# Kernel tuning notes

Measured on AMD Instinct MI355X. Metric: run time of the kernel, lower is better.

## Reference

```python
import jax, jax.numpy as jnp
import numpy as np

MARGIN = 0.36
ALPHA_INIT = 0.0
ALPHA_MOMENT = 0.995
LAMBDA_CLEAN = 1.0
LAMBDA_ADV = 1.0
EPS_SIM = 0.01
BIG = 99999.0

CNT = 8192
DIM = 128


def dot_to_dist(dot, alpha, eps=1e-12):
    return alpha * (1.0 - dot) + (1.0 - alpha) * jnp.sqrt(2.0 * (1.0 - dot) + eps)


def find_hard_negatives(dmat):
    # HyNet-style mining: dmat[i, j] = 'distance' between a_i and p_j.
    # Positive pair is the diagonal; hardest negative for triplet i is the min
    # over row i (a_i vs other p) or column i (p_i vs other a), diag excluded.
    cnt = dmat.shape[0]
    dm = dmat + jnp.eye(cnt, dtype=dmat.dtype) * BIG  # mask diagonal
    row_min = dm.min(axis=1)
    row_arg = jnp.argmin(dm, axis=1)
    col_min = dm.min(axis=0)
    col_arg = jnp.argmin(dm, axis=0)
    idx_a = jnp.arange(cnt)
    idx_p = idx_a + cnt
    # indices into cat([a, p]): hardest p lives at j+cnt, hardest a at j
    idx_n = jnp.where(row_min < col_min, row_arg + cnt, col_arg)
    return idx_a, idx_p, idx_n


def estimate_alpha(dots, labels, weights):
    # Vectorized over the 200-point alpha grid (original: Python loop).
    alphas = jnp.arange(-1.0, 1.0, 0.01, dtype=dots.dtype)  # [K=200]
    one_minus = (1.0 - dots)[None, :]                        # [1, N]
    sq = jnp.sqrt(2.0 * (1.0 - dots) + 1e-12)[None, :]       # [1, N]
    dists = alphas[:, None] * one_minus + (1.0 - alphas)[:, None] * sq  # [K, N]
    n = dists.shape[1]
    mean = dists.mean(axis=1, keepdims=True)
    std = jnp.sqrt(((dists - mean) ** 2).sum(axis=1, keepdims=True) / (n - 1))  # unbiased, as torch.std
    probs = jax.nn.sigmoid(-(dists - mean) / std)
    bce = jnp.mean(-labels * jnp.log(probs) * weights
                   - (1.0 - labels) * jnp.log(1.0 - probs) * weights, axis=1)  # [K]
    return alphas[jnp.argmin(bce)]


def _rowdot(x, y):
    return jnp.sum(x * y, axis=1)


def setup_inputs() -> dict:
    key = jax.random.key(0)
    k1, k2, k3 = jax.random.split(key, 3)
    descs = jax.random.normal(k1, (6 * CNT, DIM), dtype=jnp.float32)
    l_a_adv = jax.random.uniform(k2, (CNT,), dtype=jnp.float32)
    l_p_adv = jax.random.uniform(k3, (CNT,), dtype=jnp.float32)
    return {"descs": descs, "l_a_adv": l_a_adv, "l_p_adv": l_p_adv}


def reference(descs, l_a_adv, l_p_adv):
    cnt = descs.shape[0] // 6
    xn = descs / jnp.linalg.norm(descs, axis=1, keepdims=True)
    a     = xn[0 * cnt:1 * cnt]
    p     = xn[1 * cnt:2 * cnt]
    a_rec = xn[2 * cnt:3 * cnt]
    p_rec = xn[3 * cnt:4 * cnt]
    a_adv = xn[4 * cnt:5 * cnt]
    p_adv = xn[5 * cnt:6 * cnt]

    # hard-negative mining (no_grad in original)
    sg = jax.lax.stop_gradient
    smat_ap   = sg(a)     @ sg(p).T       # [cnt, cnt]
    smat_arpa = sg(a_rec) @ sg(p_adv).T
    smat_aapr = sg(a_adv) @ sg(p_rec).T
    idx_a, idx_p, idx_n                = find_hard_negatives(1.0 / smat_ap + EPS_SIM)
    idx_a_arpa, idx_p_arpa, idx_n_arpa = find_hard_negatives(1.0 / smat_arpa + EPS_SIM)
    idx_a_aapr, idx_p_aapr, idx_n_aapr = find_hard_negatives(1.0 / smat_aapr + EPS_SIM)

    xn_ap   = jnp.concatenate([a, p], axis=0)
    xn_arpa = jnp.concatenate([a_rec, p_adv], axis=0)
    xn_aapr = jnp.concatenate([a_adv, p_rec], axis=0)

    pos_ap   = _rowdot(xn_ap[idx_a],        xn_ap[idx_p])
    neg_ap   = _rowdot(xn_ap[idx_a],        xn_ap[idx_n])
    pos_arpa = _rowdot(xn_arpa[idx_a_arpa], xn_arpa[idx_p_arpa])
    neg_arpa = _rowdot(xn_arpa[idx_a_arpa], xn_arpa[idx_n_arpa])
    pos_aapr = _rowdot(xn_aapr[idx_a_aapr], xn_aapr[idx_p_aapr])
    neg_aapr = _rowdot(xn_aapr[idx_a_aapr], xn_aapr[idx_n_aapr])

    acos = lambda d: jnp.arccos(jnp.clip(d, -1.0, 1.0))
    mask = (MARGIN + acos(pos_ap) - acos(neg_ap) > 0).astype(descs.dtype)

    # alpha estimation (no_grad)
    dots = sg(jnp.concatenate([pos_ap, pos_arpa, pos_aapr, neg_ap, neg_arpa, neg_aapr]))
    labels = jnp.concatenate([jnp.ones(cnt * 3, descs.dtype), jnp.zeros(cnt * 3, descs.dtype)])
    weights = jnp.concatenate([
        jnp.full((cnt,), LAMBDA_CLEAN, descs.dtype), jnp.full((2 * cnt,), LAMBDA_ADV, descs.dtype),
        jnp.full((cnt,), LAMBDA_CLEAN, descs.dtype), jnp.full((2 * cnt,), LAMBDA_ADV, descs.dtype)])
    alpha_opt = estimate_alpha(dots, labels, weights)
    alpha = ALPHA_INIT * ALPHA_MOMENT + alpha_opt * (1.0 - ALPHA_MOMENT)

    loss_triplet_clean = jnp.mean((dot_to_dist(pos_ap, alpha) - dot_to_dist(neg_ap, alpha)) * mask) * LAMBDA_CLEAN
    loss_triplet_arpa = jnp.mean((l_p_adv * dot_to_dist(pos_arpa, alpha) - dot_to_dist(neg_arpa, alpha)) * mask) * LAMBDA_ADV
    loss_triplet_aapr = jnp.mean((l_a_adv * dot_to_dist(pos_aapr, alpha) - dot_to_dist(neg_aapr, alpha)) * mask) * LAMBDA_ADV
    loss = jnp.mean(jnp.stack([loss_triplet_clean, loss_triplet_arpa, loss_triplet_aapr]))

    l_mean = (l_a_adv.mean() + l_p_adv.mean()) / 2.0
    mask_ratio = mask.sum() / cnt
    return (loss, loss_triplet_clean, loss_triplet_arpa, loss_triplet_aapr, l_mean, alpha, alpha_opt, mask_ratio)
```

## Files before the change

### kernel.cpp

```cpp
#include <hip/hip_runtime.h>
#include <stdint.h>

#define CNT 8192
#define DIM 128

typedef unsigned int u32;

#define OFF_POS     ((size_t)0)
#define OFF_NEG     (OFF_POS + (size_t)3*CNT*4)
#define OFF_ROWPART (OFF_NEG + (size_t)3*CNT*4)
#define OFF_COLPART (OFF_ROWPART + (size_t)3*64*CNT*4)
#define OFF_RNORM   (OFF_COLPART + (size_t)3*64*CNT*4)
#define OFF_U       (OFF_RNORM + (size_t)6*CNT*4)
#define OFF_V       (OFF_U + (size_t)6*CNT*4)
#define OFF_MPART   (OFF_V + (size_t)6*CNT*4)
#define OFF_PSUM    (OFF_MPART + (size_t)4096)
#define OFF_XNB     (OFF_PSUM + (size_t)192*200*4)

typedef __attribute__((ext_vector_type(8))) short short8;
typedef __attribute__((ext_vector_type(4))) float f32x4;

__device__ __forceinline__ float fract1(float x){
#if __has_builtin(__builtin_amdgcn_fractf)
  return __builtin_amdgcn_fractf(x);
#else
  return x - floorf(x);
#endif
}
__device__ __forceinline__ u32 umax2(u32 a, u32 b){ return a > b ? a : b; }
__device__ __forceinline__ u32 umax3(u32 a, u32 b, u32 c){ u32 t = a > b ? a : b; return t > c ? t : c; }
__device__ __forceinline__ u32 umin2(u32 a, u32 b){ return a < b ? a : b; }

__device__ __forceinline__ float block_sum(float x, float* red, int tid){
  #pragma unroll
  for (int m=1;m<64;m<<=1) x += __shfl_xor(x, m, 64);
  if ((tid & 63) == 0) red[tid>>6] = x;
  __syncthreads();
  const float r = red[0]+red[1]+red[2]+red[3];
  __syncthreads();
  return r;
}

__global__ __launch_bounds__(256) void knorm(const float* __restrict__ in,
                                             unsigned int* __restrict__ xnb32,
                                             float* __restrict__ rnorm){
  const int row  = blockIdx.x*4 + (threadIdx.x>>6);
  const int lane = threadIdx.x & 63;
  const float2 v = *(const float2*)(in + (size_t)row*DIM + lane*2);
  float ss = v.x*v.x + v.y*v.y;
  #pragma unroll
  for (int m=1;m<64;m<<=1) ss += __shfl_xor(ss, m, 64);
  const float rn = 1.0f / sqrtf(ss);
  const float sc = ((row & CNT) ? 1.0f : 0.25f) * rn;
  unsigned int ux = __float_as_uint(v.x*sc), uy = __float_as_uint(v.y*sc);
  ux = (ux + 0x7FFFu + ((ux>>16)&1u)) >> 16;
  uy = (uy + 0x7FFFu + ((uy>>16)&1u)) >> 16;
  xnb32[(size_t)row*64 + lane] = ux | (uy<<16);
  if (lane == 0) rnorm[row] = rn;
}

__global__ __launch_bounds__(256) void kgemm(const unsigned short* __restrict__ xnb,
    u32* __restrict__ rowpart, u32* __restrict__ colpart){
  __shared__ __align__(16) unsigned short S[4][128*32];
  const int pair = blockIdx.z;
  const int xo3[3] = {0, 2*CNT, 4*CNT};
  const int yo3[3] = {CNT, 5*CNT, 3*CNT};
  const unsigned short* __restrict__ X = xnb + (size_t)xo3[pair]*DIM;
  const unsigned short* __restrict__ Y = xnb + (size_t)yo3[pair]*DIM;
  const int brow = blockIdx.y*128, bcol = blockIdx.x*128;
  const int tid = threadIdx.x, lane = tid & 63, wid = tid >> 6;
  const int wr = wid >> 1, wc = wid & 1;
  const int lrow = lane & 15, kgrp = lane >> 4;

  const int j0 = wid*2, j1 = wid*2 + 1;
  const int r0 = j0*16 + (lane>>2), r1 = j1*16 + (lane>>2);
  const int slog = (lane&3) ^ ((lane>>3)&3);
  const unsigned short* gx0 = X + (size_t)(brow + r0)*DIM + slog*8;
  const unsigned short* gx1 = X + (size_t)(brow + r1)*DIM + slog*8;
  const unsigned short* gy0 = Y + (size_t)(bcol + r0)*DIM + slog*8;
  const unsigned short* gy1 = Y + (size_t)(bcol + r1)*DIM + slog*8;

#define STAGEC(c) do{ \
    unsigned short* LX = S[((c)&1)*2]; \
    unsigned short* LY = S[((c)&1)*2 + 1]; \
    __builtin_amdgcn_global_load_lds((const __attribute__((address_space(1))) void*)(gx0 + (c)*32), \
        (__attribute__((address_space(3))) void*)(LX + j0*512), 16, 0, 0); \
    __builtin_amdgcn_global_load_lds((const __attribute__((address_space(1))) void*)(gx1 + (c)*32), \
        (__attribute__((address_space(3))) void*)(LX + j1*512), 16, 0, 0); \
    __builtin_amdgcn_global_load_lds((const __attribute__((address_space(1))) void*)(gy0 + (c)*32), \
        (__attribute__((address_space(3))) void*)(LY + j0*512), 16, 0, 0); \
    __builtin_amdgcn_global_load_lds((const __attribute__((address_space(1))) void*)(gy1 + (c)*32), \
        (__attribute__((address_space(3))) void*)(LY + j1*512), 16, 0, 0); \
  }while(0)

  f32x4 acc[4][4];
  #pragma unroll
  for (int m=0;m<4;m++)
    #pragma unroll
    for (int n=0;n<4;n++)
      acc[m][n] = (f32x4){0.f,0.f,0.f,0.f};

  STAGEC(0);
  __syncthreads();

  const int swzb = ((lrow>>1)&3) << 4;
  #pragma unroll
  for (int c=0;c<4;c++){
    if (c<3) STAGEC(c+1);
    const char* LX = (const char*)S[(c&1)*2];
    const char* LY = (const char*)S[(c&1)*2 + 1];
    const int kb = (kgrp*16) ^ swzb;
    short8 av[4], bv[4];
    #pragma unroll
    for (int m=0;m<4;m++){
      av[m] = *(const short8*)(LX + (wr*64 + m*16 + lrow)*64 + kb);
      bv[m] = *(const short8*)(LY + (wc*64 + m*16 + lrow)*64 + kb);
    }
    #pragma unroll
    for (int m=0;m<4;m++)
      #pragma unroll
      for (int n=0;n<4;n++)
        acc[m][n] = __builtin_amdgcn_mfma_f32_16x16x32_bf16(av[m], bv[n], acc[m][n], 0, 0, 0);
    if (c<3) __syncthreads();
  }

  if (blockIdx.x == blockIdx.y && wr == wc && kgrp == (lrow >> 2)){
    #pragma unroll
    for (int r=0;r<4;r++)
      if ((lrow & 3) == r){
        #pragma unroll
        for (int m=0;m<4;m++) acc[m][m][r] = 0.0f;
      }
  }

  const int colb_loc = wc*64 + lrow;
  u32 orvr[4];
  #pragma unroll
  for (int n=0;n<4;n++) orvr[n] = (u32)(127 - colb_loc - n*16);

  u32 pkc[4] = {0u,0u,0u,0u};
  u32 rpk[16];
  #pragma unroll
  for (int m=0;m<4;m++){
    #pragma unroll
    for (int r=0;r<4;r++){
      const u32 orvc = (u32)(63 - (m*16 + kgrp*4 + r));
      u32 kb2[4];
      #pragma unroll
      for (int n=0;n<4;n++)
        kb2[n] = __float_as_uint(fract1(acc[m][n][r]));
      const u32 b0 = (kb2[0] & 0xFFFFFF80u) | orvr[0];
      const u32 b1 = (kb2[1] & 0xFFFFFF80u) | orvr[1];
      const u32 b2 = (kb2[2] & 0xFFFFFF80u) | orvr[2];
      const u32 b3 = (kb2[3] & 0xFFFFFF80u) | orvr[3];
      rpk[m*4+r] = umax2(umax3(b0, b1, b2), b3);
      pkc[0] = umax2(pkc[0], (kb2[0] & 0xFFFFFFC0u) | orvc);
      pkc[1] = umax2(pkc[1], (kb2[1] & 0xFFFFFFC0u) | orvc);
      pkc[2] = umax2(pkc[2], (kb2[2] & 0xFFFFFFC0u) | orvc);
      pkc[3] = umax2(pkc[3], (kb2[3] & 0xFFFFFFC0u) | orvc);
    }
  }

  #pragma unroll
  for (int n=0;n<4;n++){
    u32 o = (u32)__shfl_xor((int)pkc[n], 16, 64); pkc[n] = umax2(pkc[n], o);
    o = (u32)__shfl_xor((int)pkc[n], 32, 64);     pkc[n] = umax2(pkc[n], o);
  }

  __syncthreads();
  u32* rowbuf = (u32*)S;
  u32* colred = (u32*)((char*)S + 20480);
  {
    const int slot = wc*16 + lrow;
    #pragma unroll
    for (int m=0;m<4;m++)
      #pragma unroll
      for (int r=0;r<4;r++){
        const int row = wr*64 + m*16 + kgrp*4 + r;
        rowbuf[row*36 + slot] = rpk[m*4+r];
      }
    if (kgrp == 0){
      #pragma unroll
      for (int n=0;n<4;n++)
        colred[wr*128 + wc*64 + n*16 + lrow] = pkc[n];
    }
  }
  __syncthreads();

  if (tid < 128){
    const u32* base = rowbuf + tid*36;
    u32 best = 0u;
    #pragma unroll
    for (int q=0;q<8;q++){
      const uint4 t = *(const uint4*)(base + q*4);
      best = umax2(best, umax2(umax3(t.x, t.y, t.z), t.w));
    }
    const int colg = 127 - (int)(best & 127u);
    rowpart[((size_t)pair*64 + blockIdx.x)*CNT + (brow + tid)] =
        ((~best) & 0xFFFFE000u) | (u32)(bcol + colg);
  } else {
    const int c = tid - 128;
    const u32 a0 = colred[c], a1 = colred[128 + c];
    const u32 w = umax2(a0, a1);
    const int rloc = (a1 > a0 ? 64 : 0) + (63 - (int)(w & 63u));
    colpart[((size_t)pair*64 + blockIdx.y)*CNT + (bcol + c)] =
        ((~w) & 0xFFFFE000u) | (u32)(brow + rloc);
  }
#undef STAGEC
}

__global__ __launch_bounds__(256) void kpickred(const float* __restrict__ descs,
    const float* __restrict__ rnorm,
    const u32* __restrict__ rowpart, const u32* __restrict__ colpart,
    float* __restrict__ pos, float* __restrict__ neg,
    float* __restrict__ u, float* __restrict__ v, float* __restrict__ mpart){
  __shared__ u32 scr[4][128];
  __shared__ u32 rvs[128], cvs[128];
  __shared__ float sred[4][5];
  const int tid = threadIdx.x, w = tid>>6, lane = tid&63;
  const int b = blockIdx.x;
  const int p = b >> 6, ibase = (b & 63) << 7;
  const int xo[3] = {0, 2*CNT, 4*CNT};
  const int yo[3] = {CNT, 5*CNT, 3*CNT};

  uint2 mn = {0xFFFFFFFFu, 0xFFFFFFFFu};
  #pragma unroll 4
  for (int t=0;t<16;t++){
    const int bxi = w*16 + t;
    const uint2 vv = *(const uint2*)(rowpart + ((size_t)p*64 + bxi)*CNT + ibase + lane*2);
    mn.x = umin2(mn.x, vv.x); mn.y = umin2(mn.y, vv.y);
  }
  scr[w][lane*2] = mn.x; scr[w][lane*2+1] = mn.y;
  __syncthreads();
  if (tid < 128)
    rvs[tid] = umin2(umin2(scr[0][tid], scr[1][tid]), umin2(scr[2][tid], scr[3][tid]));
  __syncthreads();
  mn.x = 0xFFFFFFFFu; mn.y = 0xFFFFFFFFu;
  #pragma unroll 4
  for (int t=0;t<16;t++){
    const int byi = w*16 + t;
    const uint2 vv = *(const uint2*)(colpart + ((size_t)p*64 + byi)*CNT + ibase + lane*2);
    mn.x = umin2(mn.x, vv.x); mn.y = umin2(mn.y, vv.y);
  }
  scr[w][lane*2] = mn.x; scr[w][lane*2+1] = mn.y;
  __syncthreads();
  if (tid < 128)
    cvs[tid] = umin2(umin2(scr[0][tid], scr[1][tid]), umin2(scr[2][tid], scr[3][tid]));
  __syncthreads();

  float s0=0.f, s1=0.f, s2=0.f, s3=0.f, s4=0.f;
  #pragma unroll 2
  for (int j=0;j<32;j++){
    const int il = w*32 + j;
    const int i = ibase + il;
    const u32 rv = rvs[il], cv = cvs[il];
    int orow;
    if ((rv & 0xFFFFE000u) < (cv & 0xFFFFE000u)) orow = yo[p] + (int)(rv & 0x1FFFu);
    else                                          orow = xo[p] + (int)(cv & 0x1FFFu);
    const float2 va = *(const float2*)(descs + (size_t)(xo[p]+i)*DIM + lane*2);
    const float2 vp = *(const float2*)(descs + (size_t)(yo[p]+i)*DIM + lane*2);
    const float2 vn = *(const float2*)(descs + (size_t)orow*DIM + lane*2);
    float sap = va.x*vp.x + va.y*vp.y;
    float san = va.x*vn.x + va.y*vn.y;
    #pragma unroll
    for (int m=1;m<64;m<<=1){
      sap += __shfl_xor(sap, m, 64);
      san += __shfl_xor(san, m, 64);
    }
    if (lane == 0){
      const float rna = rnorm[xo[p]+i];
      const float dp = sap * rna * rnorm[yo[p]+i];
      const float dn = san * rna * rnorm[orow];
      pos[p*CNT + i] = dp; neg[p*CNT + i] = dn;
      const float omp_ = 1.f - dp, sqp = sqrtf(2.f*omp_ + 1e-12f), up = omp_ - sqp;
      const float omn_ = 1.f - dn, sqn = sqrtf(2.f*omn_ + 1e-12f), un = omn_ - sqn;
      u[p*CNT + i] = up;           v[p*CNT + i] = sqp;
      u[3*CNT + p*CNT + i] = un;   v[3*CNT + p*CNT + i] = sqn;
      const float cup = up + 0.35f, cvp = sqp - 0.80f;
      const float cun = un + 0.35f, cvn = sqn - 0.80f;
      s0 += up + un;
      s1 += sqp + sqn;
      s2 += cup*cup + cun*cun;
      s3 += cup*cvp + cun*cvn;
      s4 += cvp*cvp + cvn*cvn;
    }
  }
  if (lane == 0){ sred[w][0]=s0; sred[w][1]=s1; sred[w][2]=s2; sred[w][3]=s3; sred[w][4]=s4; }
  __syncthreads();
  if (tid < 5)
    mpart[b*5 + tid] = sred[0][tid] + sred[1][tid] + sred[2][tid] + sred[3][tid];
}

__global__ __launch_bounds__(256) void kbce(const float* __restrict__ u, const float* __restrict__ v,
    const float* __restrict__ mpart, float* __restrict__ psum){
  __shared__ float red[4];
  __shared__ float lu[256], lv[256];
  const int tid = threadIdx.x, b = blockIdx.x;
  lu[tid] = u[b*256 + tid];
  lv[tid] = v[b*256 + tid];
  float a0=0.f,a1=0.f,a2=0.f,a3=0.f,a4=0.f;
  if (tid < 192){
    const float* mp = mpart + (size_t)tid*5;
    a0=mp[0]; a1=mp[1]; a2=mp[2]; a3=mp[3]; a4=mp[4];
  }
  a0 = block_sum(a0, red, tid);
  a1 = block_sum(a1, red, tid);
  a2 = block_sum(a2, red, tid);
  a3 = block_sum(a3, red, tid);
  a4 = block_sum(a4, red, tid);
  if (tid < 200){
    const float N = 49152.0f;
    const float mu_u = a0/N, mu_v = a1/N;
    const float du = mu_u + 0.35f, dv = mu_v - 0.80f;
    const float Suu = a2 - N*du*du;
    const float Suv = a3 - N*du*dv;
    const float Svv = a4 - N*dv*dv;
    const float a = -1.0f + 0.01f*(float)tid;
    const float mean = a*mu_u + mu_v;
    const float istd = 1.0f / sqrtf((a*a*Suu + 2.0f*a*Suv + Svv) / 49151.0f);
    const float sgn = (b < 96) ? 1.0f : -1.0f;
    const float zi = istd*sgn;
    const float zm = mean*zi;
    float s = 0.0f;
    #pragma unroll 8
    for (int j=0;j<256;j++){
      const float z = fmaf(fmaf(a, lu[j], lv[j]), zi, -zm);
      s += fmaxf(z, 0.0f) + __logf(1.0f + __expf(-fabsf(z)));
    }
    psum[b*200 + tid] = s;
  }
}

__global__ __launch_bounds__(256) void kfinal(const float* __restrict__ pos, const float* __restrict__ neg,
    const float* __restrict__ psum, const float* __restrict__ l_a_adv, const float* __restrict__ l_p_adv,
    float* __restrict__ out){
  __shared__ float sbce[200];
  __shared__ float sal[2];
  __shared__ float red[4];
  const int tid = threadIdx.x;
  if (tid < 200){
    float s = 0.f;
    for (int b=0;b<192;b++) s += psum[b*200 + tid];
    sbce[tid] = s;
  }
  __syncthreads();
  if (tid == 0){
    float best = sbce[0]; int bk = 0;
    for (int k=1;k<200;k++){
      const float vv = sbce[k];
      if (vv < best){ best = vv; bk = k; }
    }
    const float aopt = -1.0f + 0.01f*(float)bk;
    sal[0] = aopt;
    sal[1] = aopt * 0.005f;
  }
  __syncthreads();
  const float alpha = sal[1];

  float sc=0.f, sar=0.f, saa=0.f, sm=0.f, sla=0.f, slp=0.f;
  for (int i = tid; i < CNT; i += 256){
    const float pap = pos[i],        nap = neg[i];
    const float par = pos[CNT+i],    nar = neg[CNT+i];
    const float paa = pos[2*CNT+i],  naa = neg[2*CNT+i];
    const float cp = fminf(fmaxf(pap, -1.0f), 1.0f);
    const float cn = fminf(fmaxf(nap, -1.0f), 1.0f);
    const float m = (0.36f + acosf(cp) - acosf(cn) > 0.0f) ? 1.0f : 0.0f;
    #define DDIST(d) (alpha*(1.0f-(d)) + (1.0f-alpha)*sqrtf(2.0f*(1.0f-(d)) + 1e-12f))
    sc  += (DDIST(pap) - DDIST(nap)) * m;
    sar += (l_p_adv[i]*DDIST(par) - DDIST(nar)) * m;
    saa += (l_a_adv[i]*DDIST(paa) - DDIST(naa)) * m;
    sm  += m;
    sla += l_a_adv[i];
    slp += l_p_adv[i];
  }
  float vals[6] = {sc, sar, saa, sm, sla, slp};
  float tot[6];
  for (int vv=0; vv<6; vv++){
    tot[vv] = block_sum(vals[vv], red, tid);
  }
  if (tid == 0){
    const float lc  = tot[0] / (float)CNT;
    const float lar = tot[1] / (float)CNT;
    const float laa = tot[2] / (float)CNT;
    out[0] = (lc + lar + laa) / 3.0f;
    out[1] = lc;
    out[2] = lar;
    out[3] = laa;
    out[4] = (tot[4]/(float)CNT + tot[5]/(float)CNT) * 0.5f;
    out[5] = sal[1];
    out[6] = sal[0];
    out[7] = tot[3] / (float)CNT;
  }
}

extern "C" void kernel_launch(void* const* d_in, const int* in_sizes, int n_in,
                              void* d_out, int out_size, void* d_ws, size_t ws_size,
                              hipStream_t stream) {
  const float* descs = (const float*)d_in[0];
  const float* l_a   = (const float*)d_in[1];
  const float* l_p   = (const float*)d_in[2];
  float* out = (float*)d_out;
  char* ws = (char*)d_ws;

  float* pos = (float*)(ws + OFF_POS);
  float* neg = (float*)(ws + OFF_NEG);
  u32* rowpart = (u32*)(ws + OFF_ROWPART);
  u32* colpart = (u32*)(ws + OFF_COLPART);
  float* rnorm = (float*)(ws + OFF_RNORM);
  float* u     = (float*)(ws + OFF_U);
  float* v     = (float*)(ws + OFF_V);
  float* mpart = (float*)(ws + OFF_MPART);
  float* psum  = (float*)(ws + OFF_PSUM);
  unsigned int* xnb32 = (unsigned int*)(ws + OFF_XNB);
  const unsigned short* xnb = (const unsigned short*)(ws + OFF_XNB);

  knorm    <<<(6*CNT)/4, 256, 0, stream>>>(descs, xnb32, rnorm);
  kgemm    <<<dim3(64,64,3), 256, 0, stream>>>(xnb, rowpart, colpart);
  kpickred <<<192, 256, 0, stream>>>(descs, rnorm, rowpart, colpart, pos, neg, u, v, mpart);
  kbce     <<<192, 256, 0, stream>>>(u, v, mpart, psum);
  kfinal   <<<1, 256, 0, stream>>>(pos, neg, psum, l_a, l_p, out);
}
```

Baseline: 172.7 us.

## Reduce hard-negative partials with global atomicMin instead of partial buffers

The GEMM epilogue now folds each tile's per-row and per-column packed minima straight into final arrays using atomicMin, replacing the 64-way partial buffers that a second kernel had to reduce. The pick kernel is reshaped to one wavefront per triplet across 6144 blocks, and the BCE kernel sums the larger set of moment partials. This removes about 12 MB of partial writes and reads plus a reduction pass, at the cost of a memset launch, atomic contention (64 updates per address), and more per-block partials to sum in every kbce block.

```diff
diff --git a/kernel.cpp b/kernel.cpp
--- a/kernel.cpp
+++ b/kernel.cpp
@@ -8,13 +8,13 @@
 
 #define OFF_POS     ((size_t)0)
 #define OFF_NEG     (OFF_POS + (size_t)3*CNT*4)
-#define OFF_ROWPART (OFF_NEG + (size_t)3*CNT*4)
-#define OFF_COLPART (OFF_ROWPART + (size_t)3*64*CNT*4)
-#define OFF_RNORM   (OFF_COLPART + (size_t)3*64*CNT*4)
+#define OFF_FINROW  (OFF_NEG + (size_t)3*CNT*4)
+#define OFF_FINCOL  (OFF_FINROW + (size_t)3*CNT*4)
+#define OFF_RNORM   (OFF_FINCOL + (size_t)3*CNT*4)
 #define OFF_U       (OFF_RNORM + (size_t)6*CNT*4)
 #define OFF_V       (OFF_U + (size_t)6*CNT*4)
 #define OFF_MPART   (OFF_V + (size_t)6*CNT*4)
-#define OFF_PSUM    (OFF_MPART + (size_t)4096)
+#define OFF_PSUM    (OFF_MPART + (size_t)6144*5*4)
 #define OFF_XNB     (OFF_PSUM + (size_t)192*200*4)
 
 typedef __attribute__((ext_vector_type(8))) short short8;
@@ -29,7 +29,6 @@
 }
 __device__ __forceinline__ u32 umax2(u32 a, u32 b){ return a > b ? a : b; }
 __device__ __forceinline__ u32 umax3(u32 a, u32 b, u32 c){ u32 t = a > b ? a : b; return t > c ? t : c; }
-__device__ __forceinline__ u32 umin2(u32 a, u32 b){ return a < b ? a : b; }
 
 __device__ __forceinline__ float block_sum(float x, float* red, int tid){
   #pragma unroll
@@ -60,7 +59,7 @@
 }
 
 __global__ __launch_bounds__(256) void kgemm(const unsigned short* __restrict__ xnb,
-    u32* __restrict__ rowpart, u32* __restrict__ colpart){
+    u32* __restrict__ finrow, u32* __restrict__ fincol){
   __shared__ __align__(16) unsigned short S[4][128*32];
   const int pair = blockIdx.z;
   const int xo3[3] = {0, 2*CNT, 4*CNT};
@@ -196,99 +195,66 @@
       best = umax2(best, umax2(umax3(t.x, t.y, t.z), t.w));
     }
     const int colg = 127 - (int)(best & 127u);
-    rowpart[((size_t)pair*64 + blockIdx.x)*CNT + (brow + tid)] =
-        ((~best) & 0xFFFFE000u) | (u32)(bcol + colg);
+    atomicMin(&finrow[(size_t)pair*CNT + (brow + tid)],
+              ((~best) & 0xFFFFE000u) | (u32)(bcol + colg));
   } else {
     const int c = tid - 128;
     const u32 a0 = colred[c], a1 = colred[128 + c];
     const u32 w = umax2(a0, a1);
     const int rloc = (a1 > a0 ? 64 : 0) + (63 - (int)(w & 63u));
-    colpart[((size_t)pair*64 + blockIdx.y)*CNT + (bcol + c)] =
-        ((~w) & 0xFFFFE000u) | (u32)(brow + rloc);
+    atomicMin(&fincol[(size_t)pair*CNT + (bcol + c)],
+              ((~w) & 0xFFFFE000u) | (u32)(brow + rloc));
   }
 #undef STAGEC
 }
 
-__global__ __launch_bounds__(256) void kpickred(const float* __restrict__ descs,
+__global__ __launch_bounds__(256) void kpick(const float* __restrict__ descs,
     const float* __restrict__ rnorm,
-    const u32* __restrict__ rowpart, const u32* __restrict__ colpart,
+    const u32* __restrict__ finrow, const u32* __restrict__ fincol,
     float* __restrict__ pos, float* __restrict__ neg,
     float* __restrict__ u, float* __restrict__ v, float* __restrict__ mpart){
-  __shared__ u32 scr[4][128];
-  __shared__ u32 rvs[128], cvs[128];
   __shared__ float sred[4][5];
-  const int tid = threadIdx.x, w = tid>>6, lane = tid&63;
-  const int b = blockIdx.x;
-  const int p = b >> 6, ibase = (b & 63) << 7;
+  const int tid = threadIdx.x;
+  const int w4 = tid >> 6, lane = tid & 63;
+  const int e = blockIdx.x*4 + w4;
+  const int p = e >> 13, i = e & (CNT-1);
   const int xo[3] = {0, 2*CNT, 4*CNT};
   const int yo[3] = {CNT, 5*CNT, 3*CNT};
-
-  uint2 mn = {0xFFFFFFFFu, 0xFFFFFFFFu};
-  #pragma unroll 4
-  for (int t=0;t<16;t++){
-    const int bxi = w*16 + t;
-    const uint2 vv = *(const uint2*)(rowpart + ((size_t)p*64 + bxi)*CNT + ibase + lane*2);
-    mn.x = umin2(mn.x, vv.x); mn.y = umin2(mn.y, vv.y);
-  }
-  scr[w][lane*2] = mn.x; scr[w][lane*2+1] = mn.y;
-  __syncthreads();
-  if (tid < 128)
-    rvs[tid] = umin2(umin2(scr[0][tid], scr[1][tid]), umin2(scr[2][tid], scr[3][tid]));
-  __syncthreads();
-  mn.x = 0xFFFFFFFFu; mn.y = 0xFFFFFFFFu;
-  #pragma unroll 4
-  for (int t=0;t<16;t++){
-    const int byi = w*16 + t;
-    const uint2 vv = *(const uint2*)(colpart + ((size_t)p*64 + byi)*CNT + ibase + lane*2);
-    mn.x = umin2(mn.x, vv.x); mn.y = umin2(mn.y, vv.y);
-  }
-  scr[w][lane*2] = mn.x; scr[w][lane*2+1] = mn.y;
-  __syncthreads();
-  if (tid < 128)
-    cvs[tid] = umin2(umin2(scr[0][tid], scr[1][tid]), umin2(scr[2][tid], scr[3][tid]));
-  __syncthreads();
-
-  float s0=0.f, s1=0.f, s2=0.f, s3=0.f, s4=0.f;
-  #pragma unroll 2
-  for (int j=0;j<32;j++){
-    const int il = w*32 + j;
-    const int i = ibase + il;
-    const u32 rv = rvs[il], cv = cvs[il];
-    int orow;
-    if ((rv & 0xFFFFE000u) < (cv & 0xFFFFE000u)) orow = yo[p] + (int)(rv & 0x1FFFu);
-    else                                          orow = xo[p] + (int)(cv & 0x1FFFu);
-    const float2 va = *(const float2*)(descs + (size_t)(xo[p]+i)*DIM + lane*2);
-    const float2 vp = *(const float2*)(descs + (size_t)(yo[p]+i)*DIM + lane*2);
-    const float2 vn = *(const float2*)(descs + (size_t)orow*DIM + lane*2);
-    float sap = va.x*vp.x + va.y*vp.y;
-    float san = va.x*vn.x + va.y*vn.y;
-    #pragma unroll
-    for (int m=1;m<64;m<<=1){
-      sap += __shfl_xor(sap, m, 64);
-      san += __shfl_xor(san, m, 64);
-    }
-    if (lane == 0){
-      const float rna = rnorm[xo[p]+i];
-      const float dp = sap * rna * rnorm[yo[p]+i];
-      const float dn = san * rna * rnorm[orow];
-      pos[p*CNT + i] = dp; neg[p*CNT + i] = dn;
-      const float omp_ = 1.f - dp, sqp = sqrtf(2.f*omp_ + 1e-12f), up = omp_ - sqp;
-      const float omn_ = 1.f - dn, sqn = sqrtf(2.f*omn_ + 1e-12f), un = omn_ - sqn;
-      u[p*CNT + i] = up;           v[p*CNT + i] = sqp;
-      u[3*CNT + p*CNT + i] = un;   v[3*CNT + p*CNT + i] = sqn;
-      const float cup = up + 0.35f, cvp = sqp - 0.80f;
-      const float cun = un + 0.35f, cvn = sqn - 0.80f;
-      s0 += up + un;
-      s1 += sqp + sqn;
-      s2 += cup*cup + cun*cun;
-      s3 += cup*cvp + cun*cvn;
-      s4 += cvp*cvp + cvn*cvn;
-    }
-  }
-  if (lane == 0){ sred[w][0]=s0; sred[w][1]=s1; sred[w][2]=s2; sred[w][3]=s3; sred[w][4]=s4; }
+  const u32 rv = finrow[(size_t)p*CNT + i];
+  const u32 cv = fincol[(size_t)p*CNT + i];
+  int orow;
+  if ((rv & 0xFFFFE000u) < (cv & 0xFFFFE000u)) orow = yo[p] + (int)(rv & 0x1FFFu);
+  else                                          orow = xo[p] + (int)(cv & 0x1FFFu);
+  const float2 va = *(const float2*)(descs + (size_t)(xo[p]+i)*DIM + lane*2);
+  const float2 vp = *(const float2*)(descs + (size_t)(yo[p]+i)*DIM + lane*2);
+  const float2 vn = *(const float2*)(descs + (size_t)orow*DIM + lane*2);
+  float sap = va.x*vp.x + va.y*vp.y;
+  float san = va.x*vn.x + va.y*vn.y;
+  #pragma unroll
+  for (int m=1;m<64;m<<=1){
+    sap += __shfl_xor(sap, m, 64);
+    san += __shfl_xor(san, m, 64);
+  }
+  if (lane == 0){
+    const float rna = rnorm[xo[p]+i];
+    const float dp = sap * rna * rnorm[yo[p]+i];
+    const float dn = san * rna * rnorm[orow];
+    pos[p*CNT + i] = dp; neg[p*CNT + i] = dn;
+    const float omp_ = 1.f - dp, sqp = sqrtf(2.f*omp_ + 1e-12f), up = omp_ - sqp;
+    const float omn_ = 1.f - dn, sqn = sqrtf(2.f*omn_ + 1e-12f), un = omn_ - sqn;
+    u[p*CNT + i] = up;           v[p*CNT + i] = sqp;
+    u[3*CNT + p*CNT + i] = un;   v[3*CNT + p*CNT + i] = sqn;
+    const float cup = up + 0.35f, cvp = sqp - 0.80f;
+    const float cun = un + 0.35f, cvn = sqn - 0.80f;
+    sred[w4][0] = up + un;
+    sred[w4][1] = sqp + sqn;
+    sred[w4][2] = cup*cup + cun*cun;
+    sred[w4][3] = cup*cvp + cun*cvn;
+    sred[w4][4] = cvp*cvp + cvn*cvn;
+  }
   __syncthreads();
   if (tid < 5)
-    mpart[b*5 + tid] = sred[0][tid] + sred[1][tid] + sred[2][tid] + sred[3][tid];
+    mpart[blockIdx.x*5 + tid] = sred[0][tid] + sred[1][tid] + sred[2][tid] + sred[3][tid];
 }
 
 __global__ __launch_bounds__(256) void kbce(const float* __restrict__ u, const float* __restrict__ v,
@@ -299,9 +265,9 @@
   lu[tid] = u[b*256 + tid];
   lv[tid] = v[b*256 + tid];
   float a0=0.f,a1=0.f,a2=0.f,a3=0.f,a4=0.f;
-  if (tid < 192){
-    const float* mp = mpart + (size_t)tid*5;
-    a0=mp[0]; a1=mp[1]; a2=mp[2]; a3=mp[3]; a4=mp[4];
+  for (int i = tid; i < 6144; i += 256){
+    const float* mp = mpart + (size_t)i*5;
+    a0+=mp[0]; a1+=mp[1]; a2+=mp[2]; a3+=mp[3]; a4+=mp[4];
   }
   a0 = block_sum(a0, red, tid);
   a1 = block_sum(a1, red, tid);
@@ -404,8 +370,8 @@
 
   float* pos = (float*)(ws + OFF_POS);
   float* neg = (float*)(ws + OFF_NEG);
-  u32* rowpart = (u32*)(ws + OFF_ROWPART);
-  u32* colpart = (u32*)(ws + OFF_COLPART);
+  u32* finrow  = (u32*)(ws + OFF_FINROW);
+  u32* fincol  = (u32*)(ws + OFF_FINCOL);
   float* rnorm = (float*)(ws + OFF_RNORM);
   float* u     = (float*)(ws + OFF_U);
   float* v     = (float*)(ws + OFF_V);
@@ -414,9 +380,11 @@
   unsigned int* xnb32 = (unsigned int*)(ws + OFF_XNB);
   const unsigned short* xnb = (const unsigned short*)(ws + OFF_XNB);
 
-  knorm    <<<(6*CNT)/4, 256, 0, stream>>>(descs, xnb32, rnorm);
-  kgemm    <<<dim3(64,64,3), 256, 0, stream>>>(xnb, rowpart, colpart);
-  kpickred <<<192, 256, 0, stream>>>(descs, rnorm, rowpart, colpart, pos, neg, u, v, mpart);
-  kbce     <<<192, 256, 0, stream>>>(u, v, mpart, psum);
-  kfinal   <<<1, 256, 0, stream>>>(pos, neg, psum, l_a, l_p, out);
-}
+  hipMemsetAsync(finrow, 0xFF, (size_t)2*3*CNT*4, stream);
+
+  knorm  <<<(6*CNT)/4, 256, 0, stream>>>(descs, xnb32, rnorm);
+  kgemm  <<<dim3(64,64,3), 256, 0, stream>>>(xnb, finrow, fincol);
+  kpick  <<<(3*CNT)/4, 256, 0, stream>>>(descs, rnorm, finrow, fincol, pos, neg, u, v, mpart);
+  kbce   <<<192, 256, 0, stream>>>(u, v, mpart, psum);
+  kfinal <<<1, 256, 0, stream>>>(pos, neg, psum, l_a, l_p, out);
+}
```

Measured after the change: 159.4 us. 1.08x faster.
